# Kernel optimization log

Hardware: AMD Instinct MI355X
Metric: run time of the kernel (lower is better)

## Reference

```python
import jax, jax.numpy as jnp
import numpy as np

CHUNK = 64   # hyperparams['chunk_size']
HEADS = 16   # hyperparams['n_heads']


def _chunk_mask(T, cs):
    # Faithful reproduction of the original (buggy) chunked mask:
    # for chunk pair with q-chunk start i and k-chunk start j, masking is applied
    # only when i >= j, with triu(diagonal = j - i + 1). Algebraically this masks
    # position (q, k) iff q_block_start >= k_block_start and
    #   (k - q) - 2*(k_block_start - q_block_start) >= 1.
    idx = jnp.arange(T)
    blk = (idx // cs) * cs  # chunk start of each position
    qb = blk[:, None]
    kb = blk[None, :]
    masked = (qb >= kb) & ((idx[None, :] - idx[:, None] - 2 * (kb - qb)) >= 1)
    return masked  # [T, T], True = set score to -inf


def setup_inputs() -> dict:
    key = jax.random.key(0)
    ks = jax.random.split(key, 6)
    B, T, C = 2, 2048, 1024
    w = 0.02  # init scale so softmax is not saturated
    return {
        "x": jax.random.normal(ks[0], (B, T, C), jnp.float32),
        "Wq": jax.random.normal(ks[1], (C, C), jnp.float32) * w,
        "bq": jnp.zeros((C,), jnp.float32),
        "Wk": jax.random.normal(ks[2], (C, C), jnp.float32) * w,
        "bk": jnp.zeros((C,), jnp.float32),
        "Wv": jax.random.normal(ks[3], (C, C), jnp.float32) * w,
        "bv": jnp.zeros((C,), jnp.float32),
        "Wo": jax.random.normal(ks[4], (C, C), jnp.float32) * w,
        "bo": jnp.zeros((C,), jnp.float32),
        "attn_scale": jnp.full((1,), 1.0 / np.sqrt(C // HEADS), jnp.float32),
    }


def reference(x, Wq, bq, Wk, bk, Wv, bv, Wo, bo, attn_scale):
    B, T, C = x.shape
    H = HEADS
    D = C // H
    # torch nn.Linear: y = x @ W.T + b
    q = (x @ Wq.T + bq).reshape(B, T, H, D)
    k = (x @ Wk.T + bk).reshape(B, T, H, D)
    v = (x @ Wv.T + bv).reshape(B, T, H, D)
    scores = jnp.einsum("bqhd,bkhd->bhqk", q, k) * attn_scale[0]
    mask = _chunk_mask(T, CHUNK)  # [T, T]
    scores = jnp.where(mask[None, None], -jnp.inf, scores)
    attn = jax.nn.softmax(scores, axis=-1)  # [B, H, T, T]
    out = jnp.einsum("bhqk,bkhd->bqhd", attn, v).reshape(B, T, C)
    return out @ Wo.T + bo
```

## Files before the change

kernel.cpp:

```cpp
#include <hip/hip_runtime.h>


typedef __attribute__((ext_vector_type(8))) short bf16x8;
typedef __attribute__((ext_vector_type(4))) float f32x4;
typedef __attribute__((ext_vector_type(4))) float float4v;
typedef __attribute__((ext_vector_type(4))) unsigned short u16x4;

__device__ __forceinline__ unsigned short f2bf(float x){
  union { float f; unsigned int u; } c; c.f = x;
  unsigned int r = c.u + 0x7FFFu + ((c.u >> 16) & 1u);
  return (unsigned short)(r >> 16);
}
__device__ __forceinline__ float bf2f(unsigned short h){
  union { unsigned int u; float f; } c; c.u = ((unsigned int)h) << 16;
  return c.f;
}
__device__ __forceinline__ f32x4 zero4(){ f32x4 v; v[0]=0.f; v[1]=0.f; v[2]=0.f; v[3]=0.f; return v; }
__device__ __forceinline__ unsigned int cvtpk(float a, float b){
  unsigned int r;
  asm("v_cvt_pk_bf16_f32 %0, %1, %2" : "=v"(r) : "v"(a), "v"(b));
  return r;
}

#define GLDS16(g, l) __builtin_amdgcn_global_load_lds( \
  (const __attribute__((address_space(1))) void*)(g), \
  (__attribute__((address_space(3))) void*)(l), 16, 0, 0)

__global__ __launch_bounds__(256) void k_prep(
    const float* __restrict__ x,
    const float* __restrict__ Wq, const float* __restrict__ Wk,
    const float* __restrict__ Wv, const float* __restrict__ Wo,
    const float* __restrict__ bq, const float* __restrict__ bk, const float* __restrict__ bv,
    unsigned short* __restrict__ xh, unsigned short* __restrict__ wh,
    float* __restrict__ bias_cat){
  const int NX = 1048576;
  const int NTOT = 2097152;
  int i = blockIdx.x * 256 + threadIdx.x;
  if (i < 3072){
    const float* bs[3] = {bq, bk, bv};
    bias_cat[i] = bs[i >> 10][i & 1023];
  }
  int stride = gridDim.x * 256;
  for (; i < NTOT; i += stride){
    float4v v;
    u16x4 h;
    if (i < NX){
      v = ((const float4v*)x)[i];
      #pragma unroll
      for (int j = 0; j < 4; ++j) h[j] = f2bf(v[j]);
      ((u16x4*)xh)[i] = h;
    } else {
      int jj = i - NX;
      const float* srcs[4] = {Wq, Wk, Wv, Wo};
      v = ((const float4v*)srcs[jj >> 18])[jj & 0x3FFFF];
      #pragma unroll
      for (int j = 0; j < 4; ++j) h[j] = f2bf(v[j]);
      ((u16x4*)wh)[jj] = h;
    }
  }
}

template<int BN, int MODE, int SPLITA>
__global__ __launch_bounds__(256) void k_gemm(
    const unsigned short* __restrict__ Ah, const unsigned short* __restrict__ Al,
    const unsigned short* __restrict__ Bh,
    const float* __restrict__ bias, const float* __restrict__ scale_p,
    unsigned short* __restrict__ oq, unsigned short* __restrict__ okk,
    unsigned short* __restrict__ ov, float* __restrict__ fo)
{
  constexpr int MF = (BN == 128) ? 4 : 2;
  constexpr int NF = 4;
  constexpr int BISS = (BN == 128) ? 2 : 1;
  constexpr int NA = SPLITA ? 2 : 1;
  __shared__ unsigned short As[NA][128*32];
  __shared__ unsigned short Bs[BN*32];

  const int tid  = threadIdx.x;
  const int wid  = tid >> 6;
  const int lane = tid & 63;
  const int l15  = lane & 15;
  const int kg   = lane >> 4;
  const int m0 = blockIdx.y * 128;
  const int n0 = blockIdx.x * BN;
  const int wrb = (BN == 128) ? (wid >> 1) * 64 : wid * 32;
  const int wcb = (BN == 128) ? (wid & 1) * 64 : 0;
  const float qs = (MODE == 0) ? scale_p[0] : 0.f;

  f32x4 acc[MF][NF];
  #pragma unroll
  for (int a = 0; a < MF; ++a)
    #pragma unroll
    for (int b = 0; b < NF; ++b) acc[a][b] = zero4();

  for (int k0 = 0; k0 < 1024; k0 += 32){
    #pragma unroll
    for (int p = 0; p < NA; ++p){
      const unsigned short* Asrc = p ? Al : Ah;
      #pragma unroll
      for (int iss = 0; iss < 2; ++iss){
        int L = iss*2048 + tid*8;
        int row = L >> 5;
        int ck = ((L >> 3) & 3) ^ ((row >> 1) & 3);
        GLDS16(Asrc + (size_t)(m0 + row)*1024 + k0 + ck*8,
               (char*)(&As[p][0]) + iss*4096 + wid*1024);
      }
    }
    #pragma unroll
    for (int iss = 0; iss < BISS; ++iss){
      int L = iss*2048 + tid*8;
      int row = L >> 5;
      int ck = ((L >> 3) & 3) ^ ((row >> 1) & 3);
      GLDS16(Bh + (size_t)(n0 + row)*1024 + k0 + ck*8,
             (char*)(&Bs[0]) + iss*4096 + wid*1024);
    }
    __syncthreads();

    bf16x8 af[MF][NA];
    #pragma unroll
    for (int mf = 0; mf < MF; ++mf){
      int r = wrb + mf*16 + l15;
      int ckpos = kg ^ ((r >> 1) & 3);
      #pragma unroll
      for (int p = 0; p < NA; ++p)
        af[mf][p] = *(const bf16x8*)((const char*)(&As[p][0]) + r*64 + ckpos*16);
    }
    #pragma unroll
    for (int nf = 0; nf < NF; ++nf){
      int r = wcb + nf*16 + l15;
      int ckpos = kg ^ ((r >> 1) & 3);
      bf16x8 bhv = *(const bf16x8*)((const char*)(&Bs[0]) + r*64 + ckpos*16);
      #pragma unroll
      for (int mf = 0; mf < MF; ++mf){
        acc[mf][nf] = __builtin_amdgcn_mfma_f32_16x16x32_bf16(af[mf][0], bhv, acc[mf][nf], 0,0,0);
        if (SPLITA)
          acc[mf][nf] = __builtin_amdgcn_mfma_f32_16x16x32_bf16(af[mf][1], bhv, acc[mf][nf], 0,0,0);
      }
    }
    __syncthreads();
  }

  #pragma unroll
  for (int mf = 0; mf < MF; ++mf){
    #pragma unroll
    for (int nf = 0; nf < NF; ++nf){
      int colg = n0 + wcb + nf*16 + l15;
      float bb = bias[colg];
      #pragma unroll
      for (int j = 0; j < 4; ++j){
        int r = m0 + wrb + mf*16 + kg*4 + j;
        float val = acc[mf][nf][j] + bb;
        if (MODE == 1){
          fo[(size_t)r*1024 + colg] = val;
        } else {
          int bi = r >> 11, tt = r & 2047;
          int mat = colg >> 10, jj = colg & 1023;
          int h = jj >> 6, d = jj & 63;
          size_t bh_ = (size_t)(bi*16 + h);
          if (mat == 0)      oq [(bh_*2048 + tt)*64 + d] = f2bf(val * qs);
          else if (mat == 1) okk[(bh_*2048 + tt)*64 + d] = f2bf(val);
          else               ov [(bh_*64 + d)*2048 + tt] = f2bf(val);
        }
      }
    }
  }
}

__global__ __launch_bounds__(256) void k_attn(
    const unsigned short* __restrict__ Qg, const unsigned short* __restrict__ Kg,
    const unsigned short* __restrict__ Vtg,
    unsigned short* __restrict__ Ohi, unsigned short* __restrict__ Olo)
{
  __shared__ unsigned short Qs[64*64];
  __shared__ unsigned short Ks[2][64*64];
  __shared__ unsigned short Vts[2][64*64];
  __shared__ unsigned short Pw[4][16*64];

  const int tid  = threadIdx.x;
  const int wid  = tid >> 6;
  const int lane = tid & 63;
  const int l15  = lane & 15;
  const int kg   = lane >> 4;
  const int qi = blockIdx.x >> 5;
  const int bh = blockIdx.x & 31;
  const size_t base = (size_t)bh * (2048*64);

  #pragma unroll
  for (int iss = 0; iss < 2; ++iss){
    int L = iss*2048 + tid*8;
    int r = L >> 6;
    int ck = ((L >> 3) & 7) ^ (r & 7);
    GLDS16(Qg  + base + (size_t)(qi*64 + r)*64 + ck*8, (char*)Qs + iss*4096 + wid*1024);
    GLDS16(Kg  + base + (size_t)(qi*64 + r)*64 + ck*8, (char*)(&Ks[0][0])  + iss*4096 + wid*1024);
    GLDS16(Vtg + base + (size_t)r*2048 + qi*64 + ck*8, (char*)(&Vts[0][0]) + iss*4096 + wid*1024);
  }
  __syncthreads();

  bf16x8 qf[2];
  {
    int rq = wid*16 + l15;
    #pragma unroll
    for (int ks = 0; ks < 2; ++ks)
      qf[ks] = *(const bf16x8*)((const char*)Qs + rq*128 + (((ks*4 + kg) ^ (rq & 7)) * 16));
  }

  f32x4 Ot[4];
  #pragma unroll
  for (int d = 0; d < 4; ++d) Ot[d] = zero4();
  float m = -1e30f, l = 0.f;
  const int qloc = wid*16 + l15;
  char* pwb = (char*)(&Pw[wid][0]) + l15*128;
  const int swz = (l15 & 7) << 4;

  for (int kb = qi; kb < 32; ++kb){
    const int buf = (kb - qi) & 1;
    if (kb + 1 < 32){
      int nb = buf ^ 1, kb2 = kb + 1;
      #pragma unroll
      for (int iss = 0; iss < 2; ++iss){
        int L = iss*2048 + tid*8;
        int r = L >> 6;
        int ck = ((L >> 3) & 7) ^ (r & 7);
        GLDS16(Kg  + base + (size_t)(kb2*64 + r)*64 + ck*8, (char*)(&Ks[nb][0])  + iss*4096 + wid*1024);
        GLDS16(Vtg + base + (size_t)r*2048 + kb2*64 + ck*8, (char*)(&Vts[nb][0]) + iss*4096 + wid*1024);
      }
    }
    f32x4 ST[4];
    #pragma unroll
    for (int nf = 0; nf < 4; ++nf) ST[nf] = zero4();
    #pragma unroll
    for (int ks = 0; ks < 2; ++ks){
      __builtin_amdgcn_s_setprio(1);
      #pragma unroll
      for (int nf = 0; nf < 4; ++nf){
        int rk = nf*16 + l15;
        bf16x8 ak = *(const bf16x8*)((const char*)(&Ks[buf][0]) + rk*128 + (((ks*4 + kg) ^ (rk & 7)) * 16));
        ST[nf] = __builtin_amdgcn_mfma_f32_16x16x32_bf16(ak, qf[ks], ST[nf], 0,0,0);
      }
      __builtin_amdgcn_s_setprio(0);
    }
    if (kb == qi){
      #pragma unroll
      for (int nf = 0; nf < 4; ++nf)
        #pragma unroll
        for (int j = 0; j < 4; ++j)
          if (nf*16 + kg*4 + j > qloc) ST[nf][j] = -1e30f;
    }
    float mx0 = fmaxf(fmaxf(ST[0][0], ST[0][1]), fmaxf(ST[0][2], ST[0][3]));
    float mx1 = fmaxf(fmaxf(ST[1][0], ST[1][1]), fmaxf(ST[1][2], ST[1][3]));
    float mx2 = fmaxf(fmaxf(ST[2][0], ST[2][1]), fmaxf(ST[2][2], ST[2][3]));
    float mx3 = fmaxf(fmaxf(ST[3][0], ST[3][1]), fmaxf(ST[3][2], ST[3][3]));
    float pmax = fmaxf(fmaxf(mx0, mx1), fmaxf(mx2, mx3));
    pmax = fmaxf(pmax, __shfl_xor(pmax, 16, 64));
    pmax = fmaxf(pmax, __shfl_xor(pmax, 32, 64));
    if (!__all(pmax <= m + 8.0f)){
      float mn = fmaxf(m, pmax);
      float fj = __expf(m - mn);
      m = mn;
      l *= fj;
      #pragma unroll
      for (int df = 0; df < 4; ++df)
        #pragma unroll
        for (int j = 0; j < 4; ++j) Ot[df][j] *= fj;
    }
    float rsn[4];
    unsigned int pk[4][2];
    #pragma unroll
    for (int nf = 0; nf < 4; ++nf){
      float p0 = __expf(ST[nf][0] - m), p1 = __expf(ST[nf][1] - m);
      float p2 = __expf(ST[nf][2] - m), p3 = __expf(ST[nf][3] - m);
      rsn[nf] = (p0 + p1) + (p2 + p3);
      pk[nf][0] = cvtpk(p0, p1);
      pk[nf][1] = cvtpk(p2, p3);
    }
    float rs = (rsn[0] + rsn[1]) + (rsn[2] + rsn[3]);
    rs += __shfl_xor(rs, 16, 64);
    rs += __shfl_xor(rs, 32, 64);
    l += rs;
    #pragma unroll
    for (int nf = 0; nf < 4; ++nf)
      *(uint2*)(pwb + ((nf*32 + kg*8) ^ swz)) = make_uint2(pk[nf][0], pk[nf][1]);
    #pragma unroll
    for (int ks = 0; ks < 2; ++ks){
      bf16x8 pa = *(const bf16x8*)(pwb + ((ks*64 + kg*16) ^ swz));
      __builtin_amdgcn_s_setprio(1);
      #pragma unroll
      for (int df = 0; df < 4; ++df){
        int rv = df*16 + l15;
        bf16x8 vb = *(const bf16x8*)((const char*)(&Vts[buf][0]) + rv*128 + (((ks*4 + kg) ^ (rv & 7)) * 16));
        Ot[df] = __builtin_amdgcn_mfma_f32_16x16x32_bf16(vb, pa, Ot[df], 0,0,0);
      }
      __builtin_amdgcn_s_setprio(0);
    }
    __syncthreads();
  }

  const int bi = bh >> 4, h = bh & 15;
  const float rinv = 1.0f / l;
  const size_t row = (size_t)(bi*2048 + qi*64 + qloc);
  #pragma unroll
  for (int df = 0; df < 4; ++df){
    int colb = h*64 + df*16 + kg*4;
    u16x4 hv, lv;
    #pragma unroll
    for (int j = 0; j < 4; ++j){
      float v = Ot[df][j] * rinv;
      unsigned short hvv = f2bf(v);
      hv[j] = hvv;
      lv[j] = f2bf(v - bf2f(hvv));
    }
    *(u16x4*)(Ohi + row*1024 + colb) = hv;
    *(u16x4*)(Olo + row*1024 + colb) = lv;
  }
}

extern "C" void kernel_launch(void* const* d_in, const int* in_sizes, int n_in,
                              void* d_out, int out_size, void* d_ws, size_t ws_size,
                              hipStream_t stream){
  const float* x  = (const float*)d_in[0];
  const float* Wq = (const float*)d_in[1];
  const float* bq = (const float*)d_in[2];
  const float* Wk = (const float*)d_in[3];
  const float* bk = (const float*)d_in[4];
  const float* Wv = (const float*)d_in[5];
  const float* bv = (const float*)d_in[6];
  const float* Wo = (const float*)d_in[7];
  const float* bo = (const float*)d_in[8];
  const float* scale = (const float*)d_in[9];
  float* out = (float*)d_out;

  char* ws = (char*)d_ws;
  const size_t MB = 1024*1024;
  unsigned short* xh  = (unsigned short*)(ws + 0*MB);
  unsigned short* wh  = (unsigned short*)(ws + 16*MB);
  unsigned short* Qb  = (unsigned short*)(ws + 32*MB);
  unsigned short* Kb  = (unsigned short*)(ws + 40*MB);
  unsigned short* Vtb = (unsigned short*)(ws + 48*MB);
  unsigned short* Ohi = (unsigned short*)(ws + 56*MB);
  unsigned short* Olo = (unsigned short*)(ws + 64*MB);
  float* bias_cat     = (float*)(ws + 72*MB);

  hipLaunchKernelGGL(k_prep, dim3(2048), dim3(256), 0, stream,
                     x, Wq, Wk, Wv, Wo, bq, bk, bv, xh, wh, bias_cat);
  hipLaunchKernelGGL((k_gemm<128,0,0>), dim3(24,32), dim3(256), 0, stream,
                     xh, (const unsigned short*)nullptr, wh, bias_cat, scale,
                     Qb, Kb, Vtb, (float*)nullptr);
  hipLaunchKernelGGL(k_attn, dim3(1024), dim3(256), 0, stream, Qb, Kb, Vtb, Ohi, Olo);
  hipLaunchKernelGGL((k_gemm<128,1,1>), dim3(8,32), dim3(256), 0, stream,
                     Ohi, Olo, wh + 3u*1048576u, bo, (const float*)nullptr,
                     (unsigned short*)nullptr, (unsigned short*)nullptr,
                     (unsigned short*)nullptr, out);
}
```

Before: 214.9 us.

## Use exp2 softmax, reuse Q LDS for P, simplify attn addressing, smaller out-proj tiles

Folds log2(e) into the Q scale so the attention softmax can use the native v_exp_f32 instead of __expf. Drops the separate P buffer by writing P into the Q tile's LDS after Q fragments are loaded into registers, which shrinks LDS use. Load and fragment addressing is precomputed with incrementing pointers to cut integer work. The output projection GEMM switches to 64x64 tiles to launch more blocks; the risk is lower per-block reuse and the correctness of the P/Q aliasing.

After: 205.9 us. 4.2% less time.

```diff
diff --git a/kernel.cpp b/kernel.cpp
--- a/kernel.cpp
+++ b/kernel.cpp
@@ -19,6 +19,11 @@
 __device__ __forceinline__ unsigned int cvtpk(float a, float b){
   unsigned int r;
   asm("v_cvt_pk_bf16_f32 %0, %1, %2" : "=v"(r) : "v"(a), "v"(b));
+  return r;
+}
+__device__ __forceinline__ float exp2x(float x){
+  float r;
+  asm("v_exp_f32 %0, %1" : "=v"(r) : "v"(x));
   return r;
 }
 
@@ -60,7 +65,7 @@
   }
 }
 
-template<int BN, int MODE, int SPLITA>
+template<int BM, int BN, int MODE, int SPLITA>
 __global__ __launch_bounds__(256) void k_gemm(
     const unsigned short* __restrict__ Ah, const unsigned short* __restrict__ Al,
     const unsigned short* __restrict__ Bh,
@@ -68,11 +73,12 @@
     unsigned short* __restrict__ oq, unsigned short* __restrict__ okk,
     unsigned short* __restrict__ ov, float* __restrict__ fo)
 {
-  constexpr int MF = (BN == 128) ? 4 : 2;
+  constexpr int MF = (BN == 128) ? (BM/32) : (BM/64);
   constexpr int NF = 4;
-  constexpr int BISS = (BN == 128) ? 2 : 1;
+  constexpr int AISS = BM/64;
+  constexpr int BISS = BN/64;
   constexpr int NA = SPLITA ? 2 : 1;
-  __shared__ unsigned short As[NA][128*32];
+  __shared__ unsigned short As[NA][BM*32];
   __shared__ unsigned short Bs[BN*32];
 
   const int tid  = threadIdx.x;
@@ -80,11 +86,11 @@
   const int lane = tid & 63;
   const int l15  = lane & 15;
   const int kg   = lane >> 4;
-  const int m0 = blockIdx.y * 128;
+  const int m0 = blockIdx.y * BM;
   const int n0 = blockIdx.x * BN;
-  const int wrb = (BN == 128) ? (wid >> 1) * 64 : wid * 32;
+  const int wrb = (BN == 128) ? (wid >> 1) * (BM/2) : wid * (BM/4);
   const int wcb = (BN == 128) ? (wid & 1) * 64 : 0;
-  const float qs = (MODE == 0) ? scale_p[0] : 0.f;
+  const float qs = (MODE == 0) ? scale_p[0] * 1.4426950408889634f : 0.f;
 
   f32x4 acc[MF][NF];
   #pragma unroll
@@ -97,7 +103,7 @@
     for (int p = 0; p < NA; ++p){
       const unsigned short* Asrc = p ? Al : Ah;
       #pragma unroll
-      for (int iss = 0; iss < 2; ++iss){
+      for (int iss = 0; iss < AISS; ++iss){
         int L = iss*2048 + tid*8;
         int row = L >> 5;
         int ck = ((L >> 3) & 3) ^ ((row >> 1) & 3);
@@ -173,7 +179,6 @@
   __shared__ unsigned short Qs[64*64];
   __shared__ unsigned short Ks[2][64*64];
   __shared__ unsigned short Vts[2][64*64];
-  __shared__ unsigned short Pw[4][16*64];
 
   const int tid  = threadIdx.x;
   const int wid  = tid >> 6;
@@ -184,60 +189,64 @@
   const int bh = blockIdx.x & 31;
   const size_t base = (size_t)bh * (2048*64);
 
-  #pragma unroll
-  for (int iss = 0; iss < 2; ++iss){
-    int L = iss*2048 + tid*8;
-    int r = L >> 6;
-    int ck = ((L >> 3) & 7) ^ (r & 7);
-    GLDS16(Qg  + base + (size_t)(qi*64 + r)*64 + ck*8, (char*)Qs + iss*4096 + wid*1024);
-    GLDS16(Kg  + base + (size_t)(qi*64 + r)*64 + ck*8, (char*)(&Ks[0][0])  + iss*4096 + wid*1024);
-    GLDS16(Vtg + base + (size_t)r*2048 + qi*64 + ck*8, (char*)(&Vts[0][0]) + iss*4096 + wid*1024);
-  }
+  const int r0 = tid >> 3;
+  const int ck = ((tid & 7) ^ (r0 & 7)) * 8;
+  const unsigned short* qp = Qg  + base + (size_t)(qi*64 + r0)*64 + ck;
+  const unsigned short* kp = Kg  + base + (size_t)(qi*64 + r0)*64 + ck;
+  const unsigned short* vp = Vtg + base + (size_t)r0*2048 + qi*64 + ck;
+
+  GLDS16(qp,         (char*)Qs  + wid*1024);
+  GLDS16(qp + 2048,  (char*)Qs  + wid*1024 + 4096);
+  GLDS16(kp,         (char*)Ks  + wid*1024);
+  GLDS16(kp + 2048,  (char*)Ks  + wid*1024 + 4096);
+  GLDS16(vp,         (char*)Vts + wid*1024);
+  GLDS16(vp + 65536, (char*)Vts + wid*1024 + 4096);
+  kp += 4096;  vp += 64;
   __syncthreads();
 
-  bf16x8 qf[2];
-  {
-    int rq = wid*16 + l15;
-    #pragma unroll
-    for (int ks = 0; ks < 2; ++ks)
-      qf[ks] = *(const bf16x8*)((const char*)Qs + rq*128 + (((ks*4 + kg) ^ (rq & 7)) * 16));
-  }
+  const int c0 = (kg ^ (l15 & 7)) << 4;
+  const int c1 = c0 ^ 64;
+  const char* qbase = (const char*)Qs + wid*2048 + l15*128;
+  char* pwb = (char*)Qs + wid*2048 + l15*128;
+  const int pws = (kg*8) ^ ((l15 & 7) << 4);
+
+  const bf16x8 qf0 = *(const bf16x8*)(qbase + c0);
+  const bf16x8 qf1 = *(const bf16x8*)(qbase + c1);
 
   f32x4 Ot[4];
   #pragma unroll
   for (int d = 0; d < 4; ++d) Ot[d] = zero4();
   float m = -1e30f, l = 0.f;
   const int qloc = wid*16 + l15;
-  char* pwb = (char*)(&Pw[wid][0]) + l15*128;
-  const int swz = (l15 & 7) << 4;
 
   for (int kb = qi; kb < 32; ++kb){
     const int buf = (kb - qi) & 1;
+    const char* ksb = (const char*)Ks  + buf*8192 + l15*128;
+    const char* vsb = (const char*)Vts + buf*8192 + l15*128;
     if (kb + 1 < 32){
-      int nb = buf ^ 1, kb2 = kb + 1;
-      #pragma unroll
-      for (int iss = 0; iss < 2; ++iss){
-        int L = iss*2048 + tid*8;
-        int r = L >> 6;
-        int ck = ((L >> 3) & 7) ^ (r & 7);
-        GLDS16(Kg  + base + (size_t)(kb2*64 + r)*64 + ck*8, (char*)(&Ks[nb][0])  + iss*4096 + wid*1024);
-        GLDS16(Vtg + base + (size_t)r*2048 + kb2*64 + ck*8, (char*)(&Vts[nb][0]) + iss*4096 + wid*1024);
-      }
+      char* dK = (char*)Ks  + (buf^1)*8192 + wid*1024;
+      char* dV = (char*)Vts + (buf^1)*8192 + wid*1024;
+      GLDS16(kp,         dK);
+      GLDS16(kp + 2048,  dK + 4096);
+      GLDS16(vp,         dV);
+      GLDS16(vp + 65536, dV + 4096);
+      kp += 4096;  vp += 64;
     }
     f32x4 ST[4];
     #pragma unroll
     for (int nf = 0; nf < 4; ++nf) ST[nf] = zero4();
-    #pragma unroll
-    for (int ks = 0; ks < 2; ++ks){
-      __builtin_amdgcn_s_setprio(1);
-      #pragma unroll
-      for (int nf = 0; nf < 4; ++nf){
-        int rk = nf*16 + l15;
-        bf16x8 ak = *(const bf16x8*)((const char*)(&Ks[buf][0]) + rk*128 + (((ks*4 + kg) ^ (rk & 7)) * 16));
-        ST[nf] = __builtin_amdgcn_mfma_f32_16x16x32_bf16(ak, qf[ks], ST[nf], 0,0,0);
-      }
-      __builtin_amdgcn_s_setprio(0);
-    }
+    __builtin_amdgcn_s_setprio(1);
+    #pragma unroll
+    for (int nf = 0; nf < 4; ++nf){
+      bf16x8 ak = *(const bf16x8*)(ksb + nf*2048 + c0);
+      ST[nf] = __builtin_amdgcn_mfma_f32_16x16x32_bf16(ak, qf0, ST[nf], 0,0,0);
+    }
+    #pragma unroll
+    for (int nf = 0; nf < 4; ++nf){
+      bf16x8 ak = *(const bf16x8*)(ksb + nf*2048 + c1);
+      ST[nf] = __builtin_amdgcn_mfma_f32_16x16x32_bf16(ak, qf1, ST[nf], 0,0,0);
+    }
+    __builtin_amdgcn_s_setprio(0);
     if (kb == qi){
       #pragma unroll
       for (int nf = 0; nf < 4; ++nf)
@@ -254,7 +263,7 @@
     pmax = fmaxf(pmax, __shfl_xor(pmax, 32, 64));
     if (!__all(pmax <= m + 8.0f)){
       float mn = fmaxf(m, pmax);
-      float fj = __expf(m - mn);
+      float fj = exp2x(m - mn);
       m = mn;
       l *= fj;
       #pragma unroll
@@ -266,8 +275,8 @@
     unsigned int pk[4][2];
     #pragma unroll
     for (int nf = 0; nf < 4; ++nf){
-      float p0 = __expf(ST[nf][0] - m), p1 = __expf(ST[nf][1] - m);
-      float p2 = __expf(ST[nf][2] - m), p3 = __expf(ST[nf][3] - m);
+      float p0 = exp2x(ST[nf][0] - m), p1 = exp2x(ST[nf][1] - m);
+      float p2 = exp2x(ST[nf][2] - m), p3 = exp2x(ST[nf][3] - m);
       rsn[nf] = (p0 + p1) + (p2 + p3);
       pk[nf][0] = cvtpk(p0, p1);
       pk[nf][1] = cvtpk(p2, p3);
@@ -278,16 +287,20 @@
     l += rs;
     #pragma unroll
     for (int nf = 0; nf < 4; ++nf)
-      *(uint2*)(pwb + ((nf*32 + kg*8) ^ swz)) = make_uint2(pk[nf][0], pk[nf][1]);
-    #pragma unroll
-    for (int ks = 0; ks < 2; ++ks){
-      bf16x8 pa = *(const bf16x8*)(pwb + ((ks*64 + kg*16) ^ swz));
+      *(uint2*)(pwb + (pws ^ (nf*32))) = make_uint2(pk[nf][0], pk[nf][1]);
+    {
+      bf16x8 pa0 = *(const bf16x8*)(qbase + c0);
+      bf16x8 pa1 = *(const bf16x8*)(qbase + c1);
       __builtin_amdgcn_s_setprio(1);
       #pragma unroll
       for (int df = 0; df < 4; ++df){
-        int rv = df*16 + l15;
-        bf16x8 vb = *(const bf16x8*)((const char*)(&Vts[buf][0]) + rv*128 + (((ks*4 + kg) ^ (rv & 7)) * 16));
-        Ot[df] = __builtin_amdgcn_mfma_f32_16x16x32_bf16(vb, pa, Ot[df], 0,0,0);
+        bf16x8 vb = *(const bf16x8*)(vsb + df*2048 + c0);
+        Ot[df] = __builtin_amdgcn_mfma_f32_16x16x32_bf16(vb, pa0, Ot[df], 0,0,0);
+      }
+      #pragma unroll
+      for (int df = 0; df < 4; ++df){
+        bf16x8 vb = *(const bf16x8*)(vsb + df*2048 + c1);
+        Ot[df] = __builtin_amdgcn_mfma_f32_16x16x32_bf16(vb, pa1, Ot[df], 0,0,0);
       }
       __builtin_amdgcn_s_setprio(0);
     }
@@ -341,11 +354,11 @@
 
   hipLaunchKernelGGL(k_prep, dim3(2048), dim3(256), 0, stream,
                      x, Wq, Wk, Wv, Wo, bq, bk, bv, xh, wh, bias_cat);
-  hipLaunchKernelGGL((k_gemm<128,0,0>), dim3(24,32), dim3(256), 0, stream,
+  hipLaunchKernelGGL((k_gemm<128,128,0,0>), dim3(24,32), dim3(256), 0, stream,
                      xh, (const unsigned short*)nullptr, wh, bias_cat, scale,
                      Qb, Kb, Vtb, (float*)nullptr);
   hipLaunchKernelGGL(k_attn, dim3(1024), dim3(256), 0, stream, Qb, Kb, Vtb, Ohi, Olo);
-  hipLaunchKernelGGL((k_gemm<128,1,1>), dim3(8,32), dim3(256), 0, stream,
+  hipLaunchKernelGGL((k_gemm<64,64,1,1>), dim3(16,64), dim3(256), 0, stream,
                      Ohi, Olo, wh + 3u*1048576u, bo, (const float*)nullptr,
                      (unsigned short*)nullptr, (unsigned short*)nullptr,
                      (unsigned short*)nullptr, out);
```
